# Kernel tuning notes

Hardware: AMD Instinct MI355X
Metric: run time of the kernel (lower is better)

## Reference

```python
import jax, jax.numpy as jnp
import numpy as np

BLOCK = 128
EPS = 1e-5

def _fp8_dequant_weight(w, s):
    # s: [out//128, in//128] per-block scales. Expand to full weight shape.
    sb = jnp.repeat(jnp.repeat(s, BLOCK, axis=0), BLOCK, axis=1)  # [out, in]
    # fake fp8 quantize: scale down, cast to e4m3, cast back, scale up
    wq = (w / sb).astype(jnp.float8_e4m3fn).astype(jnp.float32)
    return wq * sb

def _fp8_linear(x, w, s):
    return x @ _fp8_dequant_weight(w, s).T  # [N, out]

def _layernorm(h, gamma, beta):
    mu = jnp.mean(h, axis=-1, keepdims=True)
    var = jnp.mean(jnp.square(h - mu), axis=-1, keepdims=True)
    return (h - mu) * jax.lax.rsqrt(var + EPS) * gamma + beta

def setup_inputs() -> dict:
    key = jax.random.key(0)
    ks = jax.random.split(key, 4)
    H, LO, SO, N = 4096, 8192, 2048, 8192
    return {
        "x": jax.random.normal(ks[0], (N, H), dtype=jnp.float32),
        "w_a": jax.random.normal(ks[1], (LO, H), dtype=jnp.float32),
        "s_a": jnp.ones((LO // BLOCK, H // BLOCK), dtype=jnp.float32),
        "w_b": jax.random.normal(ks[2], (SO, H), dtype=jnp.float32),
        "s_b": jnp.ones((SO // BLOCK, H // BLOCK), dtype=jnp.float32),
        "w_proj": jax.random.normal(ks[3], (H, LO + SO), dtype=jnp.float32) * 0.01,
        "gamma": jnp.ones((H,), dtype=jnp.float32),
        "beta": jnp.zeros((H,), dtype=jnp.float32),
    }

def reference(x, w_a, s_a, w_b, s_b, w_proj, gamma, beta):
    a = _fp8_linear(x, w_a, s_a)          # [N, large_out]
    b = _fp8_linear(x, w_b, s_b)          # [N, small_out]
    combined = jnp.concatenate([a, b], axis=-1)
    h = combined @ w_proj.T               # [N, hidden]
    return _layernorm(h, gamma, beta)
```

## Files before the change

kernel.cpp:

```cpp
#include <hip/hip_runtime.h>


typedef unsigned int u32;
typedef unsigned short u16;
typedef __bf16 bf16x8 __attribute__((ext_vector_type(8)));
typedef float f32x4 __attribute__((ext_vector_type(4)));
typedef u16 u16x8 __attribute__((ext_vector_type(8)));

#define AS1 __attribute__((address_space(1)))
#define AS3 __attribute__((address_space(3)))
#define FENCE() asm volatile("" ::: "memory")

__device__ __forceinline__ u16 f2bf(float f) {
  u32 u = __float_as_uint(f);
  u32 r = (u + 0x7fffu + ((u >> 16) & 1u)) >> 16;
  return (u16)r;
}

__device__ __forceinline__ float q_e4m3(float v) {
  int p = __builtin_amdgcn_cvt_pk_fp8_f32(v, v, 0, false);
  return __builtin_amdgcn_cvt_f32_fp8(p, 0);
}

__device__ __forceinline__ void gload16(const void* g, void* l) {
  __builtin_amdgcn_global_load_lds((const AS1 u32*)g, (AS3 u32*)l, 16, 0, 0);
}

__global__ __launch_bounds__(256) void k_f32_to_bf16(
    const float* __restrict__ in, u16* __restrict__ out, long n) {
  long i0 = ((long)blockIdx.x * 256 + threadIdx.x) * 8;
  long stride = (long)gridDim.x * 256 * 8;
  for (long i = i0; i < n; i += stride) {
    float4 a = *(const float4*)(in + i);
    float4 b = *(const float4*)(in + i + 4);
    u16x8 o;
    o[0] = f2bf(a.x); o[1] = f2bf(a.y); o[2] = f2bf(a.z); o[3] = f2bf(a.w);
    o[4] = f2bf(b.x); o[5] = f2bf(b.y); o[6] = f2bf(b.z); o[7] = f2bf(b.w);
    *(u16x8*)(out + i) = o;
  }
}

__global__ __launch_bounds__(256) void k_quant_transpose(
    const float* __restrict__ w, const float* __restrict__ s,
    u16* __restrict__ oT, int J, int Kd, int sCols, long oStride, int oColOff) {
  __shared__ u16 tile[64][72];
  int j0 = blockIdx.x * 64;
  int k0 = blockIdx.y * 64;
  float sc = s[(j0 >> 7) * sCols + (k0 >> 7)];
  int t = threadIdx.x;
  int row = t >> 2, seg = t & 3;
  const float4* src = (const float4*)(w + (long)(j0 + row) * Kd + k0 + seg * 16);
  u16* dst = &tile[row][seg * 16];
#pragma unroll
  for (int ii = 0; ii < 4; ++ii) {
    float4 v = src[ii];
    dst[ii * 4 + 0] = f2bf(q_e4m3(v.x / sc) * sc);
    dst[ii * 4 + 1] = f2bf(q_e4m3(v.y / sc) * sc);
    dst[ii * 4 + 2] = f2bf(q_e4m3(v.z / sc) * sc);
    dst[ii * 4 + 3] = f2bf(q_e4m3(v.w / sc) * sc);
  }
  __syncthreads();
  int r = t >> 2, cs = t & 3;
  u16* op = oT + (long)(k0 + r) * oStride + oColOff + j0 + cs * 16;
  u16x8 o0, o1;
#pragma unroll
  for (int ii = 0; ii < 8; ++ii) o0[ii] = tile[cs * 16 + ii][r];
#pragma unroll
  for (int ii = 0; ii < 8; ++ii) o1[ii] = tile[cs * 16 + 8 + ii][r];
  *(u16x8*)op = o0;
  *(u16x8*)(op + 8) = o1;
}

template <bool OUT_BF16>
__global__ __launch_bounds__(512, 2) void k_gemm8(
    const u16* __restrict__ A, const u16* __restrict__ B, void* __restrict__ Cv,
    int M, int N, int K) {
  __shared__ u16 sA[2][256 * 64];
  __shared__ u16 sB[2][256 * 64];

  const int tid = threadIdx.x;
  const int lane = tid & 63;
  const int wave = tid >> 6;
  const int wr = wave >> 2, wc = wave & 3;

  const int nwg = gridDim.x;
  const int wg = blockIdx.x;
  const int wgs = (wg & 7) * (nwg >> 3) + (wg >> 3);
  const int nbn = N >> 8;
  const int m0 = (wgs / nbn) << 8;
  const int n0 = (wgs % nbn) << 8;
  const int NT = K >> 6;

  const int lrow = lane & 15;
  const int kslot = lane >> 4;
  const int st_row = lane >> 3;
  const int st_slot = lane & 7;
  const int st_src = ((st_slot ^ st_row) * 8);

  f32x4 acc[8][4] = {};

  auto stage = [&](const u16* __restrict__ G, int row0, u16* lds, int half,
                   int kt) {
#pragma unroll
    for (int r = 0; r < 2; ++r) {
      int row = half * 128 + r * 64 + wave * 8 + st_row;
      const u16* g = G + (long)(row0 + row) * K + kt * 64 + st_src;
      u16* l = lds + row * 64 + st_slot * 8;
      gload16(g, l);
    }
  };
  auto ldA = [&](const u16* sa, int mh, int m, int ks) -> bf16x8 {
    int row = wr * 128 + mh * 64 + m * 16 + lrow;
    int slot = (ks * 4 + kslot) ^ (row & 7);
    return *(const bf16x8*)(sa + row * 64 + slot * 8);
  };
  auto ldB = [&](const u16* sb, int n, int ks) -> bf16x8 {
    int row = wc * 64 + n * 16 + lrow;
    int slot = (ks * 4 + kslot) ^ (row & 7);
    return *(const bf16x8*)(sb + row * 64 + slot * 8);
  };

  stage(A, m0, sA[0], 0, 0);
  stage(A, m0, sA[0], 1, 0);
  stage(B, n0, sB[0], 0, 0);
  stage(B, n0, sB[0], 1, 0);
  if (NT > 1) {
    stage(B, n0, sB[1], 0, 1);
    stage(B, n0, sB[1], 1, 1);
  }
  asm volatile("s_waitcnt vmcnt(4)" ::: "memory");
  __builtin_amdgcn_s_barrier();
  FENCE();

  for (int t = 0; t < NT; ++t) {
    const int p = t & 1;
    const u16* sa = sA[p];
    const u16* sb = sB[p];
    u16* saN = sA[p ^ 1];
    u16* sbC = sB[p];
    bf16x8 a0[4][2], a1[4][2], bb[4][2];

#pragma unroll
    for (int m = 0; m < 4; ++m)
#pragma unroll
      for (int ks = 0; ks < 2; ++ks) a0[m][ks] = ldA(sa, 0, m, ks);
#pragma unroll
    for (int n = 0; n < 2; ++n)
#pragma unroll
      for (int ks = 0; ks < 2; ++ks) bb[n][ks] = ldB(sb, n, ks);
    if (t + 1 < NT) stage(A, m0, saN, 0, t + 1);
    FENCE();
    __builtin_amdgcn_s_barrier();
    FENCE();
    __builtin_amdgcn_s_setprio(1);
#pragma unroll
    for (int m = 0; m < 4; ++m)
#pragma unroll
      for (int n = 0; n < 2; ++n)
#pragma unroll
        for (int ks = 0; ks < 2; ++ks)
          acc[m][n] = __builtin_amdgcn_mfma_f32_16x16x32_bf16(
              a0[m][ks], bb[n][ks], acc[m][n], 0, 0, 0);
    __builtin_amdgcn_s_setprio(0);
    FENCE();
    __builtin_amdgcn_s_barrier();
    FENCE();

#pragma unroll
    for (int n = 2; n < 4; ++n)
#pragma unroll
      for (int ks = 0; ks < 2; ++ks) bb[n][ks] = ldB(sb, n, ks);
    if (t + 1 < NT) stage(A, m0, saN, 1, t + 1);
    FENCE();
    __builtin_amdgcn_s_barrier();
    FENCE();
    __builtin_amdgcn_s_setprio(1);
#pragma unroll
    for (int m = 0; m < 4; ++m)
#pragma unroll
      for (int n = 2; n < 4; ++n)
#pragma unroll
        for (int ks = 0; ks < 2; ++ks)
          acc[m][n] = __builtin_amdgcn_mfma_f32_16x16x32_bf16(
              a0[m][ks], bb[n][ks], acc[m][n], 0, 0, 0);
    __builtin_amdgcn_s_setprio(0);
    FENCE();
    __builtin_amdgcn_s_barrier();
    FENCE();

#pragma unroll
    for (int m = 0; m < 4; ++m)
#pragma unroll
      for (int ks = 0; ks < 2; ++ks) a1[m][ks] = ldA(sa, 1, m, ks);
    if (t + 2 < NT) stage(B, n0, sbC, 0, t + 2);
    FENCE();
    __builtin_amdgcn_s_barrier();
    FENCE();
    __builtin_amdgcn_s_setprio(1);
#pragma unroll
    for (int m = 0; m < 4; ++m)
#pragma unroll
      for (int n = 2; n < 4; ++n)
#pragma unroll
        for (int ks = 0; ks < 2; ++ks)
          acc[4 + m][n] = __builtin_amdgcn_mfma_f32_16x16x32_bf16(
              a1[m][ks], bb[n][ks], acc[4 + m][n], 0, 0, 0);
    __builtin_amdgcn_s_setprio(0);
    FENCE();
    __builtin_amdgcn_s_barrier();
    FENCE();

    if (t + 2 < NT) stage(B, n0, sbC, 1, t + 2);
    FENCE();
    __builtin_amdgcn_s_barrier();
    FENCE();
    __builtin_amdgcn_s_setprio(1);
#pragma unroll
    for (int m = 0; m < 4; ++m)
#pragma unroll
      for (int n = 0; n < 2; ++n)
#pragma unroll
        for (int ks = 0; ks < 2; ++ks)
          acc[4 + m][n] = __builtin_amdgcn_mfma_f32_16x16x32_bf16(
              a1[m][ks], bb[n][ks], acc[4 + m][n], 0, 0, 0);
    __builtin_amdgcn_s_setprio(0);
    FENCE();
    if (t + 2 < NT)
      asm volatile("s_waitcnt vmcnt(4)" ::: "memory");
    else
      asm volatile("s_waitcnt vmcnt(0)" ::: "memory");
    __builtin_amdgcn_s_barrier();
    FENCE();
  }

  const int rb = m0 + wr * 128 + (lane >> 4) * 4;
  const int cb = n0 + wc * 64 + lrow;
#pragma unroll
  for (int mf = 0; mf < 8; ++mf) {
#pragma unroll
    for (int r = 0; r < 4; ++r) {
      const long rowoff = (long)(rb + mf * 16 + r) * N + cb;
#pragma unroll
      for (int n = 0; n < 4; ++n) {
        if (OUT_BF16)
          ((u16*)Cv)[rowoff + n * 16] = f2bf(acc[mf][n][r]);
        else
          ((float*)Cv)[rowoff + n * 16] = acc[mf][n][r];
      }
    }
  }
}

__global__ __launch_bounds__(256) void k_layernorm(
    float* __restrict__ h, const float* __restrict__ gamma,
    const float* __restrict__ beta) {
  const int H = 4096;
  float* p = h + (long)blockIdx.x * H;
  int t = threadIdx.x;
  float4 v[4];
  float sum = 0.f, sq = 0.f;
#pragma unroll
  for (int i = 0; i < 4; ++i) {
    v[i] = ((const float4*)p)[i * 256 + t];
    sum += v[i].x + v[i].y + v[i].z + v[i].w;
    sq += v[i].x * v[i].x + v[i].y * v[i].y + v[i].z * v[i].z + v[i].w * v[i].w;
  }
#pragma unroll
  for (int off = 32; off > 0; off >>= 1) {
    sum += __shfl_down(sum, off, 64);
    sq += __shfl_down(sq, off, 64);
  }
  __shared__ float ss[4], sg[4];
  if ((t & 63) == 0) { ss[t >> 6] = sum; sg[t >> 6] = sq; }
  __syncthreads();
  sum = ss[0] + ss[1] + ss[2] + ss[3];
  sq = sg[0] + sg[1] + sg[2] + sg[3];
  float mu = sum * (1.0f / H);
  float var = sq * (1.0f / H) - mu * mu;
  float rs = rsqrtf(var + 1e-5f);
#pragma unroll
  for (int i = 0; i < 4; ++i) {
    float4 g = ((const float4*)gamma)[i * 256 + t];
    float4 b = ((const float4*)beta)[i * 256 + t];
    float4 o;
    o.x = (v[i].x - mu) * rs * g.x + b.x;
    o.y = (v[i].y - mu) * rs * g.y + b.y;
    o.z = (v[i].z - mu) * rs * g.z + b.z;
    o.w = (v[i].w - mu) * rs * g.w + b.w;
    ((float4*)p)[i * 256 + t] = o;
  }
}

extern "C" void kernel_launch(void* const* d_in, const int* in_sizes, int n_in,
                              void* d_out, int out_size, void* d_ws,
                              size_t ws_size, hipStream_t stream) {
  const float* x      = (const float*)d_in[0];
  const float* w_a    = (const float*)d_in[1];
  const float* s_a    = (const float*)d_in[2];
  const float* w_b    = (const float*)d_in[3];
  const float* s_b    = (const float*)d_in[4];
  const float* w_proj = (const float*)d_in[5];
  const float* gamma  = (const float*)d_in[6];
  const float* beta   = (const float*)d_in[7];

  const int H = 4096, LO = 8192, SO = 2048, NR = 8192;
  const int KT = LO + SO;

  char* ws = (char*)d_ws;
  u16* xb   = (u16*)(ws);
  u16* wpb  = (u16*)(ws + 0x4000000L);
  u16* wqT  = (u16*)(ws + 0x9000000L);
  u16* weff = (u16*)(ws + 0xE000000L);
  float* h  = (float*)d_out;

  k_f32_to_bf16<<<2048, 256, 0, stream>>>(x, xb, (long)NR * H);
  k_f32_to_bf16<<<2048, 256, 0, stream>>>(w_proj, wpb, (long)H * KT);

  k_quant_transpose<<<dim3(LO / 64, H / 64), 256, 0, stream>>>(
      w_a, s_a, wqT, LO, H, H / 128, (long)KT, 0);
  k_quant_transpose<<<dim3(SO / 64, H / 64), 256, 0, stream>>>(
      w_b, s_b, wqT, SO, H, H / 128, (long)KT, LO);

  k_gemm8<true><<<(H / 256) * (H / 256), 512, 0, stream>>>(
      wpb, wqT, (void*)weff, H, H, KT);

  k_gemm8<false><<<(NR / 256) * (H / 256), 512, 0, stream>>>(
      xb, weff, (void*)h, NR, H, H);

  k_layernorm<<<NR, 256, 0, stream>>>(h, gamma, beta);
}
```

Before: 770.6 us.

## Prefetch next-tile LDS fragments across iterations and cut per-iteration barriers

Restructures the GEMM main loop so that each iteration's first A and B fragments (a0, b01) are read from LDS at the end of the previous iteration, right after the closing barrier. The remaining fragment loads (b23, a1) are rescheduled to run ahead of the MFMA phases that need them. This lets five of the eight s_barrier calls per K-iteration be removed, cutting synchronisation stalls and letting LDS reads overlap MFMA work. In exchange, more fragment registers stay live at once, which raises register pressure. Correctness now depends on the new read/write ordering between the LDS stage writes and the fragment reads being safe with fewer barriers.

After: 876.9 us. +13.8%, slower.

```diff
diff --git a/kernel.cpp b/kernel.cpp
--- a/kernel.cpp
+++ b/kernel.cpp
@@ -127,10 +127,22 @@
   if (NT > 1) {
     stage(B, n0, sB[1], 0, 1);
     stage(B, n0, sB[1], 1, 1);
-  }
-  asm volatile("s_waitcnt vmcnt(4)" ::: "memory");
+    asm volatile("s_waitcnt vmcnt(4)" ::: "memory");
+  } else {
+    asm volatile("s_waitcnt vmcnt(0)" ::: "memory");
+  }
   __builtin_amdgcn_s_barrier();
   FENCE();
+
+  bf16x8 a0[4][2], b01[2][2];
+#pragma unroll
+  for (int m = 0; m < 4; ++m)
+#pragma unroll
+    for (int ks = 0; ks < 2; ++ks) a0[m][ks] = ldA(sA[0], 0, m, ks);
+#pragma unroll
+  for (int n = 0; n < 2; ++n)
+#pragma unroll
+    for (int ks = 0; ks < 2; ++ks) b01[n][ks] = ldB(sB[0], n, ks);
 
   for (int t = 0; t < NT; ++t) {
     const int p = t & 1;
@@ -138,20 +150,13 @@
     const u16* sb = sB[p];
     u16* saN = sA[p ^ 1];
     u16* sbC = sB[p];
-    bf16x8 a0[4][2], a1[4][2], bb[4][2];
-
-#pragma unroll
-    for (int m = 0; m < 4; ++m)
-#pragma unroll
-      for (int ks = 0; ks < 2; ++ks) a0[m][ks] = ldA(sa, 0, m, ks);
+    bf16x8 a1[4][2], b23[2][2];
+
 #pragma unroll
     for (int n = 0; n < 2; ++n)
 #pragma unroll
-      for (int ks = 0; ks < 2; ++ks) bb[n][ks] = ldB(sb, n, ks);
+      for (int ks = 0; ks < 2; ++ks) b23[n][ks] = ldB(sb, n + 2, ks);
     if (t + 1 < NT) stage(A, m0, saN, 0, t + 1);
-    FENCE();
-    __builtin_amdgcn_s_barrier();
-    FENCE();
     __builtin_amdgcn_s_setprio(1);
 #pragma unroll
     for (int m = 0; m < 4; ++m)
@@ -160,20 +165,17 @@
 #pragma unroll
         for (int ks = 0; ks < 2; ++ks)
           acc[m][n] = __builtin_amdgcn_mfma_f32_16x16x32_bf16(
-              a0[m][ks], bb[n][ks], acc[m][n], 0, 0, 0);
+              a0[m][ks], b01[n][ks], acc[m][n], 0, 0, 0);
     __builtin_amdgcn_s_setprio(0);
     FENCE();
     __builtin_amdgcn_s_barrier();
     FENCE();
 
 #pragma unroll
-    for (int n = 2; n < 4; ++n)
-#pragma unroll
-      for (int ks = 0; ks < 2; ++ks) bb[n][ks] = ldB(sb, n, ks);
+    for (int m = 0; m < 4; ++m)
+#pragma unroll
+      for (int ks = 0; ks < 2; ++ks) a1[m][ks] = ldA(sa, 1, m, ks);
     if (t + 1 < NT) stage(A, m0, saN, 1, t + 1);
-    FENCE();
-    __builtin_amdgcn_s_barrier();
-    FENCE();
     __builtin_amdgcn_s_setprio(1);
 #pragma unroll
     for (int m = 0; m < 4; ++m)
@@ -182,20 +184,13 @@
 #pragma unroll
         for (int ks = 0; ks < 2; ++ks)
           acc[m][n] = __builtin_amdgcn_mfma_f32_16x16x32_bf16(
-              a0[m][ks], bb[n][ks], acc[m][n], 0, 0, 0);
+              a0[m][ks], b23[n - 2][ks], acc[m][n], 0, 0, 0);
     __builtin_amdgcn_s_setprio(0);
     FENCE();
     __builtin_amdgcn_s_barrier();
     FENCE();
 
-#pragma unroll
-    for (int m = 0; m < 4; ++m)
-#pragma unroll
-      for (int ks = 0; ks < 2; ++ks) a1[m][ks] = ldA(sa, 1, m, ks);
     if (t + 2 < NT) stage(B, n0, sbC, 0, t + 2);
-    FENCE();
-    __builtin_amdgcn_s_barrier();
-    FENCE();
     __builtin_amdgcn_s_setprio(1);
 #pragma unroll
     for (int m = 0; m < 4; ++m)
@@ -204,16 +199,9 @@
 #pragma unroll
         for (int ks = 0; ks < 2; ++ks)
           acc[4 + m][n] = __builtin_amdgcn_mfma_f32_16x16x32_bf16(
-              a1[m][ks], bb[n][ks], acc[4 + m][n], 0, 0, 0);
+              a1[m][ks], b23[n - 2][ks], acc[4 + m][n], 0, 0, 0);
     __builtin_amdgcn_s_setprio(0);
-    FENCE();
-    __builtin_amdgcn_s_barrier();
-    FENCE();
-
     if (t + 2 < NT) stage(B, n0, sbC, 1, t + 2);
-    FENCE();
-    __builtin_amdgcn_s_barrier();
-    FENCE();
     __builtin_amdgcn_s_setprio(1);
 #pragma unroll
     for (int m = 0; m < 4; ++m)
@@ -222,7 +210,7 @@
 #pragma unroll
         for (int ks = 0; ks < 2; ++ks)
           acc[4 + m][n] = __builtin_amdgcn_mfma_f32_16x16x32_bf16(
-              a1[m][ks], bb[n][ks], acc[4 + m][n], 0, 0, 0);
+              a1[m][ks], b01[n][ks], acc[4 + m][n], 0, 0, 0);
     __builtin_amdgcn_s_setprio(0);
     FENCE();
     if (t + 2 < NT)
@@ -231,6 +219,18 @@
       asm volatile("s_waitcnt vmcnt(0)" ::: "memory");
     __builtin_amdgcn_s_barrier();
     FENCE();
+    if (t + 1 < NT) {
+      const u16* sa2 = sA[p ^ 1];
+      const u16* sb2 = sB[p ^ 1];
+#pragma unroll
+      for (int m = 0; m < 4; ++m)
+#pragma unroll
+        for (int ks = 0; ks < 2; ++ks) a0[m][ks] = ldA(sa2, 0, m, ks);
+#pragma unroll
+      for (int n = 0; n < 2; ++n)
+#pragma unroll
+        for (int ks = 0; ks < 2; ++ks) b01[n][ks] = ldB(sb2, n, ks);
+    }
   }
 
   const int rb = m0 + wr * 128 + (lane >> 4) * 4;
```

## Restructure GEMM main loop to prefetch next-tile B fragments and drop a barrier phase

Applied to the files above, without the earlier changes.

Reorders the four MFMA phases in the GEMM loop so the second half of the B fragments for the next tile is loaded into registers at the end of the current iteration, guarded by a vmcnt wait. This folds the former separate fifth barrier phase into the fourth, cutting barriers per iteration and overlapping LDS reads with compute. It also moves the x-to-bf16 conversion launch to just before the second GEMM. The cost is more live registers and finer vmcnt accounting that must match the stage() issue counts exactly.

Result: no change. 771.3 us (+0.1%).

```diff
diff --git a/kernel.cpp b/kernel.cpp
--- a/kernel.cpp
+++ b/kernel.cpp
@@ -127,28 +127,55 @@
   if (NT > 1) {
     stage(B, n0, sB[1], 0, 1);
     stage(B, n0, sB[1], 1, 1);
-  }
-  asm volatile("s_waitcnt vmcnt(4)" ::: "memory");
+    asm volatile("s_waitcnt vmcnt(4)" ::: "memory");
+  } else {
+    asm volatile("s_waitcnt vmcnt(0)" ::: "memory");
+  }
   __builtin_amdgcn_s_barrier();
   FENCE();
+
+  bf16x8 b1r[2][2];
+#pragma unroll
+  for (int n = 0; n < 2; ++n)
+#pragma unroll
+    for (int ks = 0; ks < 2; ++ks) b1r[n][ks] = ldB(sB[0], n + 2, ks);
 
   for (int t = 0; t < NT; ++t) {
     const int p = t & 1;
     const u16* sa = sA[p];
     const u16* sb = sB[p];
     u16* saN = sA[p ^ 1];
+    const u16* sbN = sB[p ^ 1];
     u16* sbC = sB[p];
-    bf16x8 a0[4][2], a1[4][2], bb[4][2];
-
-#pragma unroll
-    for (int m = 0; m < 4; ++m)
-#pragma unroll
-      for (int ks = 0; ks < 2; ++ks) a0[m][ks] = ldA(sa, 0, m, ks);
+    bf16x8 aT[4][2], aB[4][2], b0r[2][2];
+
+#pragma unroll
+    for (int m = 0; m < 4; ++m)
+#pragma unroll
+      for (int ks = 0; ks < 2; ++ks) aT[m][ks] = ldA(sa, 0, m, ks);
+    if (t + 1 < NT) stage(A, m0, saN, 0, t + 1);
+    FENCE();
+    __builtin_amdgcn_s_barrier();
+    FENCE();
+    __builtin_amdgcn_s_setprio(1);
+#pragma unroll
+    for (int m = 0; m < 4; ++m)
+#pragma unroll
+      for (int n = 0; n < 2; ++n)
+#pragma unroll
+        for (int ks = 0; ks < 2; ++ks)
+          acc[m][n + 2] = __builtin_amdgcn_mfma_f32_16x16x32_bf16(
+              aT[m][ks], b1r[n][ks], acc[m][n + 2], 0, 0, 0);
+    __builtin_amdgcn_s_setprio(0);
+    FENCE();
+    __builtin_amdgcn_s_barrier();
+    FENCE();
+
 #pragma unroll
     for (int n = 0; n < 2; ++n)
 #pragma unroll
-      for (int ks = 0; ks < 2; ++ks) bb[n][ks] = ldB(sb, n, ks);
-    if (t + 1 < NT) stage(A, m0, saN, 0, t + 1);
+      for (int ks = 0; ks < 2; ++ks) b0r[n][ks] = ldB(sb, n, ks);
+    if (t + 1 < NT) stage(A, m0, saN, 1, t + 1);
     FENCE();
     __builtin_amdgcn_s_barrier();
     FENCE();
@@ -160,17 +187,17 @@
 #pragma unroll
         for (int ks = 0; ks < 2; ++ks)
           acc[m][n] = __builtin_amdgcn_mfma_f32_16x16x32_bf16(
-              a0[m][ks], bb[n][ks], acc[m][n], 0, 0, 0);
+              aT[m][ks], b0r[n][ks], acc[m][n], 0, 0, 0);
     __builtin_amdgcn_s_setprio(0);
     FENCE();
     __builtin_amdgcn_s_barrier();
     FENCE();
 
 #pragma unroll
-    for (int n = 2; n < 4; ++n)
-#pragma unroll
-      for (int ks = 0; ks < 2; ++ks) bb[n][ks] = ldB(sb, n, ks);
-    if (t + 1 < NT) stage(A, m0, saN, 1, t + 1);
+    for (int m = 0; m < 4; ++m)
+#pragma unroll
+      for (int ks = 0; ks < 2; ++ks) aB[m][ks] = ldA(sa, 1, m, ks);
+    if (t + 2 < NT) stage(B, n0, sbC, 0, t + 2);
     FENCE();
     __builtin_amdgcn_s_barrier();
     FENCE();
@@ -178,21 +205,28 @@
 #pragma unroll
     for (int m = 0; m < 4; ++m)
 #pragma unroll
-      for (int n = 2; n < 4; ++n)
+      for (int n = 0; n < 2; ++n)
 #pragma unroll
         for (int ks = 0; ks < 2; ++ks)
-          acc[m][n] = __builtin_amdgcn_mfma_f32_16x16x32_bf16(
-              a0[m][ks], bb[n][ks], acc[m][n], 0, 0, 0);
+          acc[4 + m][n + 2] = __builtin_amdgcn_mfma_f32_16x16x32_bf16(
+              aB[m][ks], b1r[n][ks], acc[4 + m][n + 2], 0, 0, 0);
     __builtin_amdgcn_s_setprio(0);
     FENCE();
     __builtin_amdgcn_s_barrier();
     FENCE();
 
-#pragma unroll
-    for (int m = 0; m < 4; ++m)
-#pragma unroll
-      for (int ks = 0; ks < 2; ++ks) a1[m][ks] = ldA(sa, 1, m, ks);
-    if (t + 2 < NT) stage(B, n0, sbC, 0, t + 2);
+    if (t + 1 < NT) {
+      if (t + 2 < NT)
+        asm volatile("s_waitcnt vmcnt(6)" ::: "memory");
+      else
+        asm volatile("s_waitcnt vmcnt(4)" ::: "memory");
+      FENCE();
+#pragma unroll
+      for (int n = 0; n < 2; ++n)
+#pragma unroll
+        for (int ks = 0; ks < 2; ++ks) b1r[n][ks] = ldB(sbN, n + 2, ks);
+    }
+    if (t + 2 < NT) stage(B, n0, sbC, 1, t + 2);
     FENCE();
     __builtin_amdgcn_s_barrier();
     FENCE();
@@ -200,29 +234,11 @@
 #pragma unroll
     for (int m = 0; m < 4; ++m)
 #pragma unroll
-      for (int n = 2; n < 4; ++n)
+      for (int n = 0; n < 2; ++n)
 #pragma unroll
         for (int ks = 0; ks < 2; ++ks)
           acc[4 + m][n] = __builtin_amdgcn_mfma_f32_16x16x32_bf16(
-              a1[m][ks], bb[n][ks], acc[4 + m][n], 0, 0, 0);
-    __builtin_amdgcn_s_setprio(0);
-    FENCE();
-    __builtin_amdgcn_s_barrier();
-    FENCE();
-
-    if (t + 2 < NT) stage(B, n0, sbC, 1, t + 2);
-    FENCE();
-    __builtin_amdgcn_s_barrier();
-    FENCE();
-    __builtin_amdgcn_s_setprio(1);
-#pragma unroll
-    for (int m = 0; m < 4; ++m)
-#pragma unroll
-      for (int n = 0; n < 2; ++n)
-#pragma unroll
-        for (int ks = 0; ks < 2; ++ks)
-          acc[4 + m][n] = __builtin_amdgcn_mfma_f32_16x16x32_bf16(
-              a1[m][ks], bb[n][ks], acc[4 + m][n], 0, 0, 0);
+              aB[m][ks], b0r[n][ks], acc[4 + m][n], 0, 0, 0);
     __builtin_amdgcn_s_setprio(0);
     FENCE();
     if (t + 2 < NT)
@@ -313,9 +329,7 @@
   u16* weff = (u16*)(ws + 0xE000000L);
   float* h  = (float*)d_out;
 
-  k_f32_to_bf16<<<2048, 256, 0, stream>>>(x, xb, (long)NR * H);
   k_f32_to_bf16<<<2048, 256, 0, stream>>>(w_proj, wpb, (long)H * KT);
-
   k_quant_transpose<<<dim3(LO / 64, H / 64), 256, 0, stream>>>(
       w_a, s_a, wqT, LO, H, H / 128, (long)KT, 0);
   k_quant_transpose<<<dim3(SO / 64, H / 64), 256, 0, stream>>>(
@@ -324,6 +338,8 @@
   k_gemm8<true><<<(H / 256) * (H / 256), 512, 0, stream>>>(
       wpb, wqT, (void*)weff, H, H, KT);
 
+  k_f32_to_bf16<<<2048, 256, 0, stream>>>(x, xb, (long)NR * H);
+
   k_gemm8<false><<<(NR / 256) * (H / 256), 512, 0, stream>>>(
       xb, weff, (void*)h, NR, H, H);
 
```
